# Optimization experiments

Measured on AMD Instinct MI355X. Metric: run time of the kernel, lower is better.

## Reference

```python
import jax, jax.numpy as jnp
import numpy as np
from jax import lax

N, C, H, W = 16, 512, 64, 64
INTER, HEADS, GROUPS, K = 512, 64, 8, 7
HEAD_DIM = INTER // HEADS


def setup_inputs() -> dict:
    key = jax.random.key(0)
    ks = jax.random.split(key, 12)
    s = 0.02
    return {
        "x": jax.random.normal(ks[0], (N, C, H, W), jnp.float32),
        "conv_w": jax.random.normal(ks[1], (INTER, C // GROUPS, K, K), jnp.float32) * s,
        "conv_b": jax.random.normal(ks[2], (INTER,), jnp.float32) * s,
        "ln_g": jnp.ones((INTER,), jnp.float32),
        "ln_b": jnp.zeros((INTER,), jnp.float32),
        "qw": jax.random.normal(ks[3], (INTER, INTER), jnp.float32) * s,
        "qb": jax.random.normal(ks[4], (INTER,), jnp.float32) * s,
        "kw": jax.random.normal(ks[5], (INTER, INTER), jnp.float32) * s,
        "kb": jax.random.normal(ks[6], (INTER,), jnp.float32) * s,
        "vw": jax.random.normal(ks[7], (INTER, INTER), jnp.float32) * s,
        "vb": jax.random.normal(ks[8], (INTER,), jnp.float32) * s,
        "pw": jax.random.normal(ks[9], (C, INTER), jnp.float32) * s,
        "pb": jax.random.normal(ks[10], (C,), jnp.float32) * s,
        "beta": jax.random.normal(ks[11], (1,), jnp.float32),
    }


def reference(x, conv_w, conv_b, ln_g, ln_b, qw, qb, kw, kb, vw, vb, pw, pb, beta):
    n, c, h, w = x.shape
    hw = h * w
    pad = (K - 1) // 2
    # grouped conv, NCHW
    xc = lax.conv_general_dilated(
        x, conv_w, window_strides=(1, 1), padding=[(pad, pad), (pad, pad)],
        dimension_numbers=("NCHW", "OIHW", "NCHW"), feature_group_count=GROUPS)
    xc = xc + conv_b[None, :, None, None]
    xc = xc.reshape(n, INTER, hw).transpose(0, 2, 1)  # [N, HW, INTER]
    # LayerNorm over channel dim
    mu = jnp.mean(xc, axis=-1, keepdims=True)
    var = jnp.mean(jnp.square(xc - mu), axis=-1, keepdims=True)
    xn = (xc - mu) * lax.rsqrt(var + 1e-5) * ln_g + ln_b
    # projections (torch Linear: y = x @ W.T + b)
    q = (xn @ qw.T + qb).reshape(n, hw, HEADS, HEAD_DIM).transpose(0, 2, 1, 3)  # [N,h,HW,d]
    k = (xn @ kw.T + kb).reshape(n, hw, HEADS, HEAD_DIM).transpose(0, 2, 3, 1)  # [N,h,d,HW]
    v = (xn @ vw.T + vb).reshape(n, hw, HEADS, HEAD_DIM).transpose(0, 2, 1, 3)  # [N,h,HW,d]
    k = jax.nn.softmax(k, axis=3)  # softmax over tokens
    corr = jnp.einsum("nhds,nhse->nhde", k, v)      # [N,h,d,d] compact context
    atten = jnp.einsum("nhsd,nhde->nhse", q, corr)  # [N,h,HW,d]
    atten = atten.transpose(0, 2, 1, 3).reshape(n, hw, INTER)
    xa = (atten @ pw.T + pb).transpose(0, 2, 1).reshape(n, c, h, w)
    return beta[0] * xa + x
```

## Files before the change

### kernel.cpp

```cpp
#include <hip/hip_runtime.h>
#include <hip/hip_bf16.h>

#define N_IMG 16
#define C_DIM 512
#define H_DIM 64
#define W_DIM 64
#define HW 4096
#define INTER 512
#define HEADS 64
#define GROUPS 8
#define KSZ 7
#define CPG 64
#define M_TOT (N_IMG * HW)

typedef short bf16x8 __attribute__((ext_vector_type(8)));
typedef short bf16x4 __attribute__((ext_vector_type(4)));
typedef float f32x4 __attribute__((ext_vector_type(4)));
typedef unsigned int u32;

__device__ __forceinline__ unsigned short f2bf(float f) {
    __hip_bfloat16 h = __float2bfloat16(f);
    return *reinterpret_cast<unsigned short*>(&h);
}
__device__ __forceinline__ float bf2f(unsigned short u) {
    u32 x = ((u32)u) << 16;
    union { u32 i; float f; } c; c.i = x; return c.f;
}
__device__ __forceinline__ void gload16(const void* g, void* l) {
    __builtin_amdgcn_global_load_lds(
        (const __attribute__((address_space(1))) u32*)g,
        (__attribute__((address_space(3))) u32*)l, 16, 0, 0);
}
__device__ __forceinline__ void raw_barrier() {
    asm volatile("" ::: "memory");
    __builtin_amdgcn_s_barrier();
    asm volatile("" ::: "memory");
}
#define WAIT_VM(N) asm volatile("s_waitcnt vmcnt(" #N ")" ::: "memory")

__global__ __launch_bounds__(256) void prep_kernel(
    const float* __restrict__ cw, const float* __restrict__ kw,
    const float* __restrict__ vw, const float* __restrict__ pw,
    const float* __restrict__ x,
    unsigned short* __restrict__ pk, unsigned short* __restrict__ kwb,
    unsigned short* __restrict__ vwb, unsigned short* __restrict__ pwb,
    float* __restrict__ crw, unsigned short* __restrict__ xb)
{
    const int b = blockIdx.x;
    const int tid = threadIdx.x;
    if (b < 6272) {
        int p = b * 256 + tid;
        int ci = p & 63;
        int co = (p >> 6) & 63;
        int r  = p >> 12;
        int dx = r % 7;
        int dyg = r / 7;
        int dy = dyg % 7;
        int g  = dyg / 7;
        float v = cw[(((size_t)(g * 64 + co)) * 64 + ci) * 49 + dy * 7 + dx];
        pk[(size_t)(g * 49 + dy * 7 + dx) * 4096 + co * 64 + (ci ^ ((co & 7) << 3))] = f2bf(v);
        return;
    }
    if (b < 8320) {
        const float* w = (b < 7296) ? kw : vw;
        unsigned short* wp = (b < 7296) ? kwb : vwb;
        int e = ((b < 7296) ? (b - 6272) : (b - 7296)) * 256 + tid;
        int j = e & 7;
        int chunk = (e >> 3) & 511;
        int kt = (e >> 12) & 15;
        int t = e >> 16;
        int col = chunk & 127, kq = chunk >> 7;
        wp[e] = f2bf(w[(size_t)(t * 128 + col) * 512 + kt * 32 + kq * 8 + j]);
        return;
    }
    if (b < 9344) {
        int i = (b - 8320) * 256 + tid;
        pwb[i] = f2bf(pw[i]);
        return;
    }
    if (b < 9632) {
        crw[(b - 9344) * 256 + tid] = 0.f;
        return;
    }
    {
        const int idx = b - 9632;
        const int n   = idx / 560;
        const int rem = idx - n * 560;
        const int g   = rem / 70;
        const int row = rem - g * 70;
        unsigned short* dst = xb + ((size_t)(n * 8 + g) * 70 + row) * 4608;

        if (row < 3 || row > 66) {
            bf16x8 z = (bf16x8){0,0,0,0,0,0,0,0};
            *(bf16x8*)&dst[tid * 8] = z;
            *(bf16x8*)&dst[(256 + tid) * 8] = z;
            if (tid < 64) *(bf16x8*)&dst[(512 + tid) * 8] = z;
            return;
        }
        const int y = row - 3;
        const int xcol = tid & 63;
        const int oct = tid >> 6;
        const int col = xcol + 3;
        const int cswz = (col & 7) << 3;
        const float* src = x + (((size_t)(n * C_DIM + g * CPG)) * H_DIM + y) * W_DIM + xcol;
#pragma unroll
        for (int h = 0; h < 2; ++h) {
            const int ci0 = oct * 16 + h * 8;
            unsigned short tmp[8];
#pragma unroll
            for (int j = 0; j < 8; ++j)
                tmp[j] = f2bf(src[(size_t)(ci0 + j) * (H_DIM * W_DIM)]);
            *(bf16x8*)&dst[col * 64 + (ci0 ^ cswz)] = *(bf16x8*)tmp;
        }
        if (tid < 64) {
            const int hc[8] = {0, 1, 2, 67, 68, 69, 70, 71};
            int c = hc[tid >> 3], o8 = (tid & 7) * 8;
            *(bf16x8*)&dst[c * 64 + (o8 ^ ((c & 7) << 3))] = (bf16x8){0,0,0,0,0,0,0,0};
        }
    }
}

__global__ __launch_bounds__(256) void conv_mfma2_kernel(
    const unsigned short* __restrict__ xb, const unsigned short* __restrict__ pk,
    const float* __restrict__ cb, unsigned short* __restrict__ xc)
{
    __shared__ __align__(16) unsigned short in_ring[4 * 72 * 64];
    __shared__ __align__(16) unsigned short w_lds[2 * 4096];

    const int bid  = blockIdx.x;
    const int wgid = (bid & 7) * 256 + (bid >> 3);
    const int g  = wgid >> 8;
    const int n  = (wgid >> 4) & 15;
    const int y0 = (wgid & 15) * 4;
    const int tid  = threadIdx.x;
    const int lane = tid & 63;
    const int wv   = tid >> 6;
    const int lx   = lane & 15;
    const int q4   = lane >> 4;
    const int koff = q4 * 8;
    const int c3   = 512 + (tid & 63);

    const unsigned short* xbase = xb + ((size_t)(n * 8 + g) * 70) * 4608;
    const unsigned short* pkg   = pk + (size_t)g * 49 * 4096;

    f32x4 acc[4][4];
#pragma unroll
    for (int i = 0; i < 4; ++i)
#pragma unroll
        for (int j = 0; j < 4; ++j) acc[i][j] = (f32x4){0.f, 0.f, 0.f, 0.f};

#pragma unroll
    for (int r = 0; r < 4; ++r) {
        const unsigned short* src = xbase + (size_t)(y0 + r) * 4608;
        gload16(src + tid * 8,         &in_ring[r * 4608 + tid * 8]);
        gload16(src + (256 + tid) * 8, &in_ring[r * 4608 + (256 + tid) * 8]);
        gload16(src + c3 * 8,          &in_ring[r * 4608 + c3 * 8]);
    }
    gload16(pkg + tid * 8,         &w_lds[tid * 8]);
    gload16(pkg + (256 + tid) * 8, &w_lds[(256 + tid) * 8]);

    for (int dy = 0; dy < 7; ++dy) {
#pragma unroll
        for (int dx = 0; dx < 7; ++dx) {
            const int t = dy * 7 + dx;
            raw_barrier();
            if (dx == 0 && dy > 0) {
                const int slot = (dy + 3) & 3;
                const unsigned short* src = xbase + (size_t)(y0 + dy + 3) * 4608;
                gload16(src + tid * 8,         &in_ring[slot * 4608 + tid * 8]);
                gload16(src + (256 + tid) * 8, &in_ring[slot * 4608 + (256 + tid) * 8]);
                gload16(src + c3 * 8,          &in_ring[slot * 4608 + c3 * 8]);
            }
            if (t < 48) {
                const unsigned short* wsrc = pkg + (size_t)(t + 1) * 4096;
                unsigned short* wdst = &w_lds[((t + 1) & 1) * 4096];
                gload16(wsrc + tid * 8,         wdst + tid * 8);
                gload16(wsrc + (256 + tid) * 8, wdst + (256 + tid) * 8);
                WAIT_VM(2);
            } else {
                WAIT_VM(0);
            }
            __builtin_amdgcn_sched_barrier(0);
            raw_barrier();
            __builtin_amdgcn_sched_barrier(0);

            __builtin_amdgcn_s_setprio(1);
            const unsigned short* wcur = &w_lds[(t & 1) * 4096];
            bf16x8 b[2][4];
#pragma unroll
            for (int kc = 0; kc < 2; ++kc)
#pragma unroll
                for (int ct = 0; ct < 4; ++ct) {
                    const int co = ct * 16 + lx;
                    b[kc][ct] = *(const bf16x8*)
                        &wcur[co * 64 + ((kc * 32 + koff) ^ ((co & 7) << 3))];
                }
            const int col  = wv * 16 + lx + dx;
            const int cswz = (col & 7) << 3;
#pragma unroll
            for (int ty = 0; ty < 4; ++ty) {
                const int slot = (dy + ty) & 3;
#pragma unroll
                for (int kc = 0; kc < 2; ++kc) {
                    bf16x8 a = *(const bf16x8*)
                        &in_ring[slot * 4608 + col * 64 + ((kc * 32 + koff) ^ cswz)];
#pragma unroll
                    for (int ct = 0; ct < 4; ++ct)
                        acc[ty][ct] = __builtin_amdgcn_mfma_f32_16x16x32_bf16(
                            a, b[kc][ct], acc[ty][ct], 0, 0, 0);
                }
            }
            __builtin_amdgcn_s_setprio(0);
        }
    }

#pragma unroll
    for (int ct = 0; ct < 4; ++ct) {
        const float bv = cb[g * 64 + ct * 16 + lx];
        const int cidx = g * 64 + ct * 16 + lx;
#pragma unroll
        for (int ty = 0; ty < 4; ++ty) {
            const int yy = y0 + ty;
#pragma unroll
            for (int r = 0; r < 4; ++r) {
                const int xx = wv * 16 + q4 * 4 + r;
                xc[((size_t)(n * HW + yy * W_DIM + xx)) * INTER + cidx]
                    = f2bf(acc[ty][ct][r] + bv);
            }
        }
    }
}

__global__ __launch_bounds__(256) void ln_kernel(
    unsigned short* __restrict__ xc, const float* __restrict__ g,
    const float* __restrict__ b)
{
    const int tid  = threadIdx.x;
    const int half = tid >> 7;
    const int l    = tid & 127;
    const size_t row = (size_t)blockIdx.x * 2 + half;

    bf16x4 u = *(const bf16x4*)(xc + row * INTER + l * 4);
    float v0 = bf2f((unsigned short)u[0]), v1 = bf2f((unsigned short)u[1]);
    float v2 = bf2f((unsigned short)u[2]), v3 = bf2f((unsigned short)u[3]);
    float s  = v0 + v1 + v2 + v3;
    float sq = v0 * v0 + v1 * v1 + v2 * v2 + v3 * v3;
#pragma unroll
    for (int off = 32; off; off >>= 1) {
        s  += __shfl_xor(s, off);
        sq += __shfl_xor(sq, off);
    }
    __shared__ float red[4][2];
    const int wid = tid >> 6;
    if ((tid & 63) == 0) { red[wid][0] = s; red[wid][1] = sq; }
    __syncthreads();
    const int w0 = half * 2;
    float S  = red[w0][0] + red[w0 + 1][0];
    float SQ = red[w0][1] + red[w0 + 1][1];
    float mu  = S * (1.f / INTER);
    float var = SQ * (1.f / INTER) - mu * mu;
    float rs  = rsqrtf(var + 1e-5f);
    float4 gg = ((const float4*)g)[l];
    float4 bb = ((const float4*)b)[l];
    bf16x4 o;
    o[0] = (short)f2bf((v0 - mu) * rs * gg.x + bb.x);
    o[1] = (short)f2bf((v1 - mu) * rs * gg.y + bb.y);
    o[2] = (short)f2bf((v2 - mu) * rs * gg.z + bb.z);
    o[3] = (short)f2bf((v3 - mu) * rs * gg.w + bb.w);
    *(bf16x4*)(xc + row * INTER + l * 4) = o;
}

__global__ __launch_bounds__(256, 2) void gemm_kv_corr_kernel(
    const unsigned short* __restrict__ A,
    const unsigned short* __restrict__ Wk, const unsigned short* __restrict__ Wv,
    const float* __restrict__ bk, const float* __restrict__ bv,
    float* __restrict__ crw, float* __restrict__ esw)
{
    __shared__ __align__(16) unsigned short pool[32768];
    unsigned short* ek_lds = pool;
    unsigned short* v_lds  = pool + 16384;

    const int tid  = threadIdx.x;
    const int lane = tid & 63;
    const int w    = tid >> 6;
    const int lx   = lane & 15;
    const int kq4  = lane >> 4;

    const int orig = blockIdx.x;
    const int wgid = (orig & 7) * 256 + (orig >> 3);
    const int m0   = (wgid >> 2) * 128;
    const int ct4  = wgid & 3;
    const int mbase = (w & 1) * 64;
    const int nbase = (w >> 1) * 64;
    const int n = m0 >> 12;

    const unsigned short* wkt = Wk + (size_t)ct4 * 65536;
    const unsigned short* wvt = Wv + (size_t)ct4 * 65536;

    f32x4 acck[4][4], accv[4][4];
#pragma unroll
    for (int i = 0; i < 4; ++i)
#pragma unroll
        for (int j = 0; j < 4; ++j) {
            acck[i][j] = (f32x4){0.f, 0.f, 0.f, 0.f};
            accv[i][j] = (f32x4){0.f, 0.f, 0.f, 0.f};
        }

#pragma unroll
    for (int it = 0; it < 2; ++it) {
        int c = it * 256 + tid;
        gload16(A + (size_t)(m0 + (c & 127)) * 512 + (c >> 7) * 8, &pool[c * 8]);
        gload16(wkt + c * 8, &pool[(1024 + c) * 8]);
        gload16(wvt + c * 8, &pool[(2048 + c) * 8]);
    }

    for (int kt = 0; kt < 16; ++kt) {
        const int b = kt & 1;
        if (kt < 15) {
            const int nb = b ^ 1;
#pragma unroll
            for (int it = 0; it < 2; ++it) {
                int c = it * 256 + tid;
                gload16(A + (size_t)(m0 + (c & 127)) * 512 + (kt + 1) * 32 + (c >> 7) * 8,
                        &pool[(nb * 512 + c) * 8]);
                gload16(wkt + (size_t)(kt + 1) * 4096 + c * 8, &pool[(1024 + nb * 512 + c) * 8]);
                gload16(wvt + (size_t)(kt + 1) * 4096 + c * 8, &pool[(2048 + nb * 512 + c) * 8]);
            }
            WAIT_VM(6);
        } else {
            WAIT_VM(0);
        }
        __builtin_amdgcn_sched_barrier(0);
        raw_barrier();
        __builtin_amdgcn_sched_barrier(0);

        __builtin_amdgcn_s_setprio(1);
        bf16x8 a[4], bkf[4], bvf[4];
#pragma unroll
        for (int i = 0; i < 4; ++i) {
            a[i]   = *(const bf16x8*)&pool[(b * 512 + kq4 * 128 + mbase + i * 16 + lx) * 8];
            bkf[i] = *(const bf16x8*)&pool[(1024 + b * 512 + kq4 * 128 + nbase + i * 16 + lx) * 8];
            bvf[i] = *(const bf16x8*)&pool[(2048 + b * 512 + kq4 * 128 + nbase + i * 16 + lx) * 8];
        }
#pragma unroll
        for (int i = 0; i < 4; ++i)
#pragma unroll
            for (int j = 0; j < 4; ++j) {
                acck[i][j] = __builtin_amdgcn_mfma_f32_16x16x32_bf16(a[i], bkf[j], acck[i][j], 0, 0, 0);
                accv[i][j] = __builtin_amdgcn_mfma_f32_16x16x32_bf16(a[i], bvf[j], accv[i][j], 0, 0, 0);
            }
        __builtin_amdgcn_s_setprio(0);
        raw_barrier();
    }

#pragma unroll
    for (int j = 0; j < 4; ++j) {
        const int colk = nbase + j * 16 + lx;
        const float bkv = bk[ct4 * 128 + colk];
        const float bvv = bv[ct4 * 128 + colk];
        const int sw = (colk & 7) << 3;
#pragma unroll
        for (int i = 0; i < 4; ++i) {
            const int t0 = mbase + i * 16 + kq4 * 4;
            const int idx = colk * 128 + (t0 ^ sw);
            bf16x4 ew, vw;
#pragma unroll
            for (int r = 0; r < 4; ++r) {
                ew[r] = (short)f2bf(__expf(acck[i][j][r] + bkv));
                vw[r] = (short)f2bf(accv[i][j][r] + bvv);
            }
            *(bf16x4*)&ek_lds[idx] = ew;
            *(bf16x4*)&v_lds[idx]  = vw;
        }
    }
    const int d = lane >> 3, e = lane & 7;
    const int hbase = (w >> 1) * 8;
#pragma unroll
    for (int h = 0; h < 8; ++h) {
        const int hb = hbase + h;
        const int ck = hb * 8 + d;
        const int ce = hb * 8 + e;
        const int swk = d << 3, swe = e << 3;
        float crh = 0.f, esh = 0.f;
#pragma unroll
        for (int tb = 0; tb < 16; ++tb) {
            const int t0 = mbase + tb * 4;
            bf16x4 ekv = *(const bf16x4*)&ek_lds[ck * 128 + (t0 ^ swk)];
            bf16x4 vvv = *(const bf16x4*)&v_lds[ce * 128 + (t0 ^ swe)];
#pragma unroll
            for (int r = 0; r < 4; ++r) {
                float ekf = bf2f((unsigned short)ekv[r]);
                crh = fmaf(ekf, bf2f((unsigned short)vvv[r]), crh);
                esh += ekf;
            }
        }
        const int nh = n * 64 + ct4 * 16 + hb;
        atomicAdd(&crw[(size_t)nh * 64 + d * 8 + e], crh);
        if (e == 0) atomicAdd(&esw[nh * 8 + d], esh);
    }
}

__global__ __launch_bounds__(256) void gcomp_kernel(
    const float* __restrict__ qw, const float* __restrict__ crw,
    const float* __restrict__ esw, unsigned short* __restrict__ G)
{
    const int h = blockIdx.x;
    const int n = blockIdx.y;
    const int tid = threadIdx.x;
    const int nh = n * 64 + h;
    __shared__ float C[64];
    if (tid < 64) C[tid] = crw[(size_t)nh * 64 + tid] / esw[nh * 8 + (tid >> 3)];
    __syncthreads();
#pragma unroll
    for (int rep = 0; rep < 2; ++rep) {
        const int k = rep * 256 + tid;
        float o[8] = {};
#pragma unroll
        for (int d = 0; d < 8; ++d) {
            float qv = qw[(size_t)(h * 8 + d) * 512 + k];
#pragma unroll
            for (int e = 0; e < 8; ++e) o[e] = fmaf(qv, C[d * 8 + e], o[e]);
        }
        bf16x8 ov;
#pragma unroll
        for (int e = 0; e < 8; ++e) ov[e] = (short)f2bf(o[e]);
        *(bf16x8*)&G[((size_t)n * 512 + k) * 512 + h * 8] = ov;
    }
}

__global__ __launch_bounds__(256) void compose_kernel(
    const unsigned short* __restrict__ Pwb, const unsigned short* __restrict__ G,
    unsigned short* __restrict__ wfp)
{
    __shared__ __align__(16) unsigned short pool[16384];
    const int tid  = threadIdx.x;
    const int lane = tid & 63;
    const int w    = tid >> 6;
    const int lx   = lane & 15;
    const int kq4  = lane >> 4;

    const int tile = blockIdx.x;
    const int n    = blockIdx.y;
    const int m0 = (tile >> 2) * 128;
    const int n0 = (tile & 3) * 128;
    const int mbase = (w & 1) * 64;
    const int nbase = (w >> 1) * 64;
    const unsigned short* Gn = G + (size_t)n * 262144;

    f32x4 acc[4][4];
#pragma unroll
    for (int i = 0; i < 4; ++i)
#pragma unroll
        for (int j = 0; j < 4; ++j) acc[i][j] = (f32x4){0.f, 0.f, 0.f, 0.f};

#pragma unroll
    for (int it = 0; it < 2; ++it) {
        int c = it * 256 + tid;
        gload16(Pwb + (size_t)(m0 + (c & 127)) * 512 + (c >> 7) * 8, &pool[c * 8]);
        gload16(Gn + (size_t)(n0 + (c & 127)) * 512 + (c >> 7) * 8, &pool[(1024 + c) * 8]);
    }
    __syncthreads();

    for (int kt = 0; kt < 16; ++kt) {
        const int b = kt & 1;
        if (kt < 15) {
            const int nb = b ^ 1;
#pragma unroll
            for (int it = 0; it < 2; ++it) {
                int c = it * 256 + tid;
                gload16(Pwb + (size_t)(m0 + (c & 127)) * 512 + (kt + 1) * 32 + (c >> 7) * 8,
                        &pool[(nb * 512 + c) * 8]);
                gload16(Gn + (size_t)(n0 + (c & 127)) * 512 + (kt + 1) * 32 + (c >> 7) * 8,
                        &pool[(1024 + nb * 512 + c) * 8]);
            }
        }
        bf16x8 a[4], bf[4];
#pragma unroll
        for (int i = 0; i < 4; ++i) {
            a[i]  = *(const bf16x8*)&pool[(b * 512 + kq4 * 128 + mbase + i * 16 + lx) * 8];
            bf[i] = *(const bf16x8*)&pool[(1024 + b * 512 + kq4 * 128 + nbase + i * 16 + lx) * 8];
        }
#pragma unroll
        for (int i = 0; i < 4; ++i)
#pragma unroll
            for (int j = 0; j < 4; ++j)
                acc[i][j] = __builtin_amdgcn_mfma_f32_16x16x32_bf16(a[i], bf[j], acc[i][j], 0, 0, 0);
        __syncthreads();
    }

    unsigned short* wfn = wfp + (size_t)n * 262144;
#pragma unroll
    for (int j = 0; j < 4; ++j) {
        const int K = n0 + nbase + j * 16 + lx;
        const int kt = K >> 5, kq = (K >> 3) & 3, jp = K & 7;
        const int ebase = (kt << 12) | (kq << 10) | jp;
#pragma unroll
        for (int i = 0; i < 4; ++i) {
            const int rowb = m0 + mbase + i * 16 + kq4 * 4;
#pragma unroll
            for (int r = 0; r < 4; ++r) {
                const int C = rowb + r;
                wfn[((C >> 7) << 16) | ebase | ((C & 127) << 3)] = f2bf(acc[i][j][r]);
            }
        }
    }
}

__global__ __launch_bounds__(256) void bias2_kernel(
    const float* __restrict__ qb, const float* __restrict__ crw,
    const float* __restrict__ esw, const float* __restrict__ pw,
    const float* __restrict__ pb, float* __restrict__ b2)
{
    const int n = blockIdx.x;
    const int tid = threadIdx.x;
    __shared__ float qbc[512];
#pragma unroll
    for (int rep = 0; rep < 2; ++rep) {
        int j = rep * 256 + tid;
        int h = j >> 3, e = j & 7;
        const int nh = n * 64 + h;
        float s = 0.f;
#pragma unroll
        for (int d = 0; d < 8; ++d)
            s += qb[h * 8 + d] * crw[(size_t)nh * 64 + d * 8 + e] / esw[nh * 8 + d];
        qbc[j] = s;
    }
    __syncthreads();
#pragma unroll
    for (int rep = 0; rep < 2; ++rep) {
        int c = rep * 256 + tid;
        const float4* pr = (const float4*)(pw + (size_t)c * 512);
        float s = pb[c];
        for (int q = 0; q < 128; ++q) {
            float4 pv = pr[q];
            s += qbc[q * 4 + 0] * pv.x + qbc[q * 4 + 1] * pv.y
               + qbc[q * 4 + 2] * pv.z + qbc[q * 4 + 3] * pv.w;
        }
        b2[n * 512 + c] = s;
    }
}

__global__ __launch_bounds__(256) void gemm_p_kernel(
    const unsigned short* __restrict__ A, const unsigned short* __restrict__ Wp,
    const float* __restrict__ bias, float* __restrict__ Y,
    const float* __restrict__ xres, const float* __restrict__ betap)
{
    __shared__ __align__(16) unsigned short pool[24576];
    const int tid  = threadIdx.x;
    const int lane = tid & 63;
    const int w    = tid >> 6;
    const int lx   = lane & 15;
    const int kq4  = lane >> 4;

    const int orig = blockIdx.x;
    const int wgid = (orig & 7) * 128 + (orig >> 3);
    const int m0 = (wgid >> 2) * 256;
    const int n0 = (wgid & 3) * 128;
    const int mbase = (w & 1) * 128;
    const int nbase = (w >> 1) * 64;
    const int nimg = m0 >> 12;

    f32x4 acc[8][4];
#pragma unroll
    for (int i = 0; i < 8; ++i)
#pragma unroll
        for (int j = 0; j < 4; ++j) acc[i][j] = (f32x4){0.f, 0.f, 0.f, 0.f};

    const unsigned short* wpt = Wp + (size_t)nimg * 262144 + (size_t)(wgid & 3) * 65536;

#pragma unroll
    for (int it = 0; it < 4; ++it) {
        int c = it * 256 + tid;
        gload16(A + (size_t)(m0 + (c & 255)) * 512 + (c >> 8) * 8, &pool[c * 8]);
    }
#pragma unroll
    for (int it = 0; it < 2; ++it) {
        int c = it * 256 + tid;
        gload16(wpt + c * 8, &pool[16384 + c * 8]);
    }

    for (int kt = 0; kt < 16; ++kt) {
        const int b = kt & 1;
        if (kt < 15) {
            const int nb = b ^ 1;
#pragma unroll
            for (int it = 0; it < 4; ++it) {
                int c = it * 256 + tid;
                gload16(A + (size_t)(m0 + (c & 255)) * 512 + (kt + 1) * 32 + (c >> 8) * 8,
                        &pool[(nb * 1024 + c) * 8]);
            }
#pragma unroll
            for (int it = 0; it < 2; ++it) {
                int c = it * 256 + tid;
                gload16(wpt + (size_t)(kt + 1) * 4096 + c * 8,
                        &pool[16384 + (nb * 512 + c) * 8]);
            }
            WAIT_VM(6);
        } else {
            WAIT_VM(0);
        }
        __builtin_amdgcn_sched_barrier(0);
        raw_barrier();
        __builtin_amdgcn_sched_barrier(0);

        __builtin_amdgcn_s_setprio(1);
        bf16x8 a[8], bf[4];
#pragma unroll
        for (int i = 0; i < 8; ++i)
            a[i] = *(const bf16x8*)&pool[(b * 1024 + kq4 * 256 + mbase + i * 16 + lx) * 8];
#pragma unroll
        for (int j = 0; j < 4; ++j)
            bf[j] = *(const bf16x8*)&pool[16384 + (b * 512 + kq4 * 128 + nbase + j * 16 + lx) * 8];
#pragma unroll
        for (int i = 0; i < 8; ++i)
#pragma unroll
            for (int j = 0; j < 4; ++j)
                acc[i][j] = __builtin_amdgcn_mfma_f32_16x16x32_bf16(a[i], bf[j], acc[i][j], 0, 0, 0);
        __builtin_amdgcn_s_setprio(0);
        raw_barrier();
    }

    const float beta = betap[0];
#pragma unroll
    for (int j = 0; j < 4; ++j) {
        const int c = n0 + nbase + j * 16 + lx;
        const float pbv = bias[nimg * 512 + c];
        const size_t cbase = ((size_t)(nimg * 512 + c)) * 4096;
#pragma unroll
        for (int i = 0; i < 8; ++i) {
            const int s = (m0 & 4095) + mbase + i * 16 + kq4 * 4;
            float4 xr = *(const float4*)(xres + cbase + s);
            float4 o;
            o.x = beta * (acc[i][j][0] + pbv) + xr.x;
            o.y = beta * (acc[i][j][1] + pbv) + xr.y;
            o.z = beta * (acc[i][j][2] + pbv) + xr.z;
            o.w = beta * (acc[i][j][3] + pbv) + xr.w;
            *(float4*)(Y + cbase + s) = o;
        }
    }
}

extern "C" void kernel_launch(void* const* d_in, const int* in_sizes, int n_in,
                              void* d_out, int out_size, void* d_ws, size_t ws_size,
                              hipStream_t stream)
{
    (void)in_sizes; (void)n_in; (void)out_size; (void)ws_size;
    const float* x   = (const float*)d_in[0];
    const float* cw  = (const float*)d_in[1];
    const float* cb  = (const float*)d_in[2];
    const float* lng = (const float*)d_in[3];
    const float* lnb = (const float*)d_in[4];
    const float* qw  = (const float*)d_in[5];
    const float* qb  = (const float*)d_in[6];
    const float* kw  = (const float*)d_in[7];
    const float* kb  = (const float*)d_in[8];
    const float* vw  = (const float*)d_in[9];
    const float* vb  = (const float*)d_in[10];
    const float* pw  = (const float*)d_in[11];
    const float* pb  = (const float*)d_in[12];
    const float* beta = (const float*)d_in[13];
    float* out = (float*)d_out;

    char* ws = (char*)d_ws;
    const size_t SZ  = (size_t)M_TOT * INTER * sizeof(float);
    const size_t HSZ = (size_t)M_TOT * INTER * 2;
    unsigned short* xc   = (unsigned short*)ws;
    unsigned short* G    = (unsigned short*)(ws + HSZ);
    unsigned short* wfp  = G + (size_t)16 * 262144;
    unsigned short* pwb  = wfp + (size_t)16 * 262144;
    float* b2            = (float*)(pwb + 262144);
    float* crw  = (float*)(ws + SZ);
    float* esw  = crw + 65536;
    unsigned short* pk  = (unsigned short*)(ws + SZ + (2 << 20));
    unsigned short* kwb = (unsigned short*)(ws + SZ + (6 << 20));
    unsigned short* vwb = kwb + 262144;
    unsigned short* xb  = vwb + 262144;

    prep_kernel<<<dim3(18592), 256, 0, stream>>>(cw, kw, vw, pw, x,
                                                 pk, kwb, vwb, pwb, crw, xb);

    conv_mfma2_kernel<<<dim3(2048), 256, 0, stream>>>(xb, pk, cb, xc);
    ln_kernel<<<dim3(M_TOT / 2), 256, 0, stream>>>(xc, lng, lnb);

    gemm_kv_corr_kernel<<<dim3(2048), 256, 0, stream>>>(xc, kwb, vwb, kb, vb, crw, esw);

    gcomp_kernel<<<dim3(64, 16), 256, 0, stream>>>(qw, crw, esw, G);
    compose_kernel<<<dim3(16, 16), 256, 0, stream>>>(pwb, G, wfp);
    bias2_kernel<<<dim3(16), 256, 0, stream>>>(qb, crw, esw, pw, pb, b2);

    gemm_p_kernel<<<dim3(1024), 256, 0, stream>>>(xc, wfp, b2, out, x, beta);
}
```

Measured before the change: 511.0 us.

## Drop setprio in MFMA loops, make LayerNorm one wave per row, merge gcomp with bias2

Removes the s_setprio raise/lower around the MFMA sections of the conv, KV-corr and projection GEMM kernels. Rewrites LayerNorm so each 64-lane wave handles one row with 16-byte loads and only a wave-level shuffle reduction, dropping the shared-memory reduction and __syncthreads. Merges bias2 into the gcomp kernel as 16 extra blocks, saving one launch and letting the two run concurrently. The risk is that the priority hint was helping wave interleaving in the GEMMs.

After: 489.3 us (median of 2 runs). -4.3%, faster.

```diff
diff --git a/kernel.cpp b/kernel.cpp
--- a/kernel.cpp
+++ b/kernel.cpp
@@ -184,7 +184,6 @@
             raw_barrier();
             __builtin_amdgcn_sched_barrier(0);
 
-            __builtin_amdgcn_s_setprio(1);
             const unsigned short* wcur = &w_lds[(t & 1) * 4096];
             bf16x8 b[2][4];
 #pragma unroll
@@ -210,7 +209,6 @@
                             a, b[kc][ct], acc[ty][ct], 0, 0, 0);
                 }
             }
-            __builtin_amdgcn_s_setprio(0);
         }
     }
 
@@ -235,39 +233,36 @@
     unsigned short* __restrict__ xc, const float* __restrict__ g,
     const float* __restrict__ b)
 {
-    const int tid  = threadIdx.x;
-    const int half = tid >> 7;
-    const int l    = tid & 127;
-    const size_t row = (size_t)blockIdx.x * 2 + half;
-
-    bf16x4 u = *(const bf16x4*)(xc + row * INTER + l * 4);
-    float v0 = bf2f((unsigned short)u[0]), v1 = bf2f((unsigned short)u[1]);
-    float v2 = bf2f((unsigned short)u[2]), v3 = bf2f((unsigned short)u[3]);
-    float s  = v0 + v1 + v2 + v3;
-    float sq = v0 * v0 + v1 * v1 + v2 * v2 + v3 * v3;
+    const int tid = threadIdx.x;
+    const size_t row = (size_t)blockIdx.x * 4 + (tid >> 6);
+    const int l = tid & 63;
+    unsigned short* p = xc + row * INTER + l * 8;
+
+    bf16x8 u = *(const bf16x8*)p;
+    float v[8];
+    float s = 0.f, sq = 0.f;
+#pragma unroll
+    for (int j = 0; j < 8; ++j) {
+        v[j] = bf2f((unsigned short)u[j]);
+        s += v[j]; sq += v[j] * v[j];
+    }
 #pragma unroll
     for (int off = 32; off; off >>= 1) {
         s  += __shfl_xor(s, off);
         sq += __shfl_xor(sq, off);
     }
-    __shared__ float red[4][2];
-    const int wid = tid >> 6;
-    if ((tid & 63) == 0) { red[wid][0] = s; red[wid][1] = sq; }
-    __syncthreads();
-    const int w0 = half * 2;
-    float S  = red[w0][0] + red[w0 + 1][0];
-    float SQ = red[w0][1] + red[w0 + 1][1];
-    float mu  = S * (1.f / INTER);
-    float var = SQ * (1.f / INTER) - mu * mu;
-    float rs  = rsqrtf(var + 1e-5f);
-    float4 gg = ((const float4*)g)[l];
-    float4 bb = ((const float4*)b)[l];
-    bf16x4 o;
-    o[0] = (short)f2bf((v0 - mu) * rs * gg.x + bb.x);
-    o[1] = (short)f2bf((v1 - mu) * rs * gg.y + bb.y);
-    o[2] = (short)f2bf((v2 - mu) * rs * gg.z + bb.z);
-    o[3] = (short)f2bf((v3 - mu) * rs * gg.w + bb.w);
-    *(bf16x4*)(xc + row * INTER + l * 4) = o;
+    const float mu  = s * (1.f / INTER);
+    const float var = sq * (1.f / INTER) - mu * mu;
+    const float rs  = rsqrtf(var + 1e-5f);
+    float4 g0 = ((const float4*)g)[l * 2], g1 = ((const float4*)g)[l * 2 + 1];
+    float4 b0 = ((const float4*)b)[l * 2], b1 = ((const float4*)b)[l * 2 + 1];
+    const float gg[8] = {g0.x, g0.y, g0.z, g0.w, g1.x, g1.y, g1.z, g1.w};
+    const float bb[8] = {b0.x, b0.y, b0.z, b0.w, b1.x, b1.y, b1.z, b1.w};
+    bf16x8 o;
+#pragma unroll
+    for (int j = 0; j < 8; ++j)
+        o[j] = (short)f2bf((v[j] - mu) * rs * gg[j] + bb[j]);
+    *(bf16x8*)p = o;
 }
 
 __global__ __launch_bounds__(256, 2) void gemm_kv_corr_kernel(
@@ -334,7 +329,6 @@
         raw_barrier();
         __builtin_amdgcn_sched_barrier(0);
 
-        __builtin_amdgcn_s_setprio(1);
         bf16x8 a[4], bkf[4], bvf[4];
 #pragma unroll
         for (int i = 0; i < 4; ++i) {
@@ -349,7 +343,6 @@
                 acck[i][j] = __builtin_amdgcn_mfma_f32_16x16x32_bf16(a[i], bkf[j], acck[i][j], 0, 0, 0);
                 accv[i][j] = __builtin_amdgcn_mfma_f32_16x16x32_bf16(a[i], bvf[j], accv[i][j], 0, 0, 0);
             }
-        __builtin_amdgcn_s_setprio(0);
         raw_barrier();
     }
 
@@ -400,31 +393,65 @@
     }
 }
 
-__global__ __launch_bounds__(256) void gcomp_kernel(
-    const float* __restrict__ qw, const float* __restrict__ crw,
-    const float* __restrict__ esw, unsigned short* __restrict__ G)
-{
-    const int h = blockIdx.x;
-    const int n = blockIdx.y;
+__global__ __launch_bounds__(256) void gcomp_bias2_kernel(
+    const float* __restrict__ qw, const float* __restrict__ qb,
+    const float* __restrict__ crw, const float* __restrict__ esw,
+    const float* __restrict__ pw, const float* __restrict__ pb,
+    unsigned short* __restrict__ G, float* __restrict__ b2)
+{
+    const int blk = blockIdx.x;
     const int tid = threadIdx.x;
-    const int nh = n * 64 + h;
-    __shared__ float C[64];
-    if (tid < 64) C[tid] = crw[(size_t)nh * 64 + tid] / esw[nh * 8 + (tid >> 3)];
-    __syncthreads();
-#pragma unroll
-    for (int rep = 0; rep < 2; ++rep) {
-        const int k = rep * 256 + tid;
-        float o[8] = {};
-#pragma unroll
-        for (int d = 0; d < 8; ++d) {
-            float qv = qw[(size_t)(h * 8 + d) * 512 + k];
-#pragma unroll
-            for (int e = 0; e < 8; ++e) o[e] = fmaf(qv, C[d * 8 + e], o[e]);
-        }
-        bf16x8 ov;
-#pragma unroll
-        for (int e = 0; e < 8; ++e) ov[e] = (short)f2bf(o[e]);
-        *(bf16x8*)&G[((size_t)n * 512 + k) * 512 + h * 8] = ov;
+    if (blk < 1024) {
+        const int h = blk & 63;
+        const int n = blk >> 6;
+        const int nh = n * 64 + h;
+        __shared__ float C[64];
+        if (tid < 64) C[tid] = crw[(size_t)nh * 64 + tid] / esw[nh * 8 + (tid >> 3)];
+        __syncthreads();
+#pragma unroll
+        for (int rep = 0; rep < 2; ++rep) {
+            const int k = rep * 256 + tid;
+            float o[8] = {};
+#pragma unroll
+            for (int d = 0; d < 8; ++d) {
+                float qv = qw[(size_t)(h * 8 + d) * 512 + k];
+#pragma unroll
+                for (int e = 0; e < 8; ++e) o[e] = fmaf(qv, C[d * 8 + e], o[e]);
+            }
+            bf16x8 ov;
+#pragma unroll
+            for (int e = 0; e < 8; ++e) ov[e] = (short)f2bf(o[e]);
+            *(bf16x8*)&G[((size_t)n * 512 + k) * 512 + h * 8] = ov;
+        }
+        return;
+    }
+    {
+        const int n = blk - 1024;
+        __shared__ float qbc[512];
+#pragma unroll
+        for (int rep = 0; rep < 2; ++rep) {
+            int j = rep * 256 + tid;
+            int h = j >> 3, e = j & 7;
+            const int nh = n * 64 + h;
+            float s = 0.f;
+#pragma unroll
+            for (int d = 0; d < 8; ++d)
+                s += qb[h * 8 + d] * crw[(size_t)nh * 64 + d * 8 + e] / esw[nh * 8 + d];
+            qbc[j] = s;
+        }
+        __syncthreads();
+#pragma unroll
+        for (int rep = 0; rep < 2; ++rep) {
+            int c = rep * 256 + tid;
+            const float4* pr = (const float4*)(pw + (size_t)c * 512);
+            float s = pb[c];
+            for (int q = 0; q < 128; ++q) {
+                float4 pv = pr[q];
+                s += qbc[q * 4 + 0] * pv.x + qbc[q * 4 + 1] * pv.y
+                   + qbc[q * 4 + 2] * pv.z + qbc[q * 4 + 3] * pv.w;
+            }
+            b2[n * 512 + c] = s;
+        }
     }
 }
 
@@ -506,40 +533,6 @@
     }
 }
 
-__global__ __launch_bounds__(256) void bias2_kernel(
-    const float* __restrict__ qb, const float* __restrict__ crw,
-    const float* __restrict__ esw, const float* __restrict__ pw,
-    const float* __restrict__ pb, float* __restrict__ b2)
-{
-    const int n = blockIdx.x;
-    const int tid = threadIdx.x;
-    __shared__ float qbc[512];
-#pragma unroll
-    for (int rep = 0; rep < 2; ++rep) {
-        int j = rep * 256 + tid;
-        int h = j >> 3, e = j & 7;
-        const int nh = n * 64 + h;
-        float s = 0.f;
-#pragma unroll
-        for (int d = 0; d < 8; ++d)
-            s += qb[h * 8 + d] * crw[(size_t)nh * 64 + d * 8 + e] / esw[nh * 8 + d];
-        qbc[j] = s;
-    }
-    __syncthreads();
-#pragma unroll
-    for (int rep = 0; rep < 2; ++rep) {
-        int c = rep * 256 + tid;
-        const float4* pr = (const float4*)(pw + (size_t)c * 512);
-        float s = pb[c];
-        for (int q = 0; q < 128; ++q) {
-            float4 pv = pr[q];
-            s += qbc[q * 4 + 0] * pv.x + qbc[q * 4 + 1] * pv.y
-               + qbc[q * 4 + 2] * pv.z + qbc[q * 4 + 3] * pv.w;
-        }
-        b2[n * 512 + c] = s;
-    }
-}
-
 __global__ __launch_bounds__(256) void gemm_p_kernel(
     const unsigned short* __restrict__ A, const unsigned short* __restrict__ Wp,
     const float* __restrict__ bias, float* __restrict__ Y,
@@ -603,7 +596,6 @@
         raw_barrier();
         __builtin_amdgcn_sched_barrier(0);
 
-        __builtin_amdgcn_s_setprio(1);
         bf16x8 a[8], bf[4];
 #pragma unroll
         for (int i = 0; i < 8; ++i)
@@ -616,7 +608,6 @@
 #pragma unroll
             for (int j = 0; j < 4; ++j)
                 acc[i][j] = __builtin_amdgcn_mfma_f32_16x16x32_bf16(a[i], bf[j], acc[i][j], 0, 0, 0);
-        __builtin_amdgcn_s_setprio(0);
         raw_barrier();
     }
 
@@ -680,13 +671,12 @@
                                                  pk, kwb, vwb, pwb, crw, xb);
 
     conv_mfma2_kernel<<<dim3(2048), 256, 0, stream>>>(xb, pk, cb, xc);
-    ln_kernel<<<dim3(M_TOT / 2), 256, 0, stream>>>(xc, lng, lnb);
+    ln_kernel<<<dim3(M_TOT / 4), 256, 0, stream>>>(xc, lng, lnb);
 
     gemm_kv_corr_kernel<<<dim3(2048), 256, 0, stream>>>(xc, kwb, vwb, kb, vb, crw, esw);
 
-    gcomp_kernel<<<dim3(64, 16), 256, 0, stream>>>(qw, crw, esw, G);
+    gcomp_bias2_kernel<<<dim3(1040), 256, 0, stream>>>(qw, qb, crw, esw, pw, pb, G, b2);
     compose_kernel<<<dim3(16, 16), 256, 0, stream>>>(pwb, G, wfp);
-    bias2_kernel<<<dim3(16), 256, 0, stream>>>(qb, crw, esw, pw, pb, b2);
 
     gemm_p_kernel<<<dim3(1024), 256, 0, stream>>>(xc, wfp, b2, out, x, beta);
 }
```
